# Performance work log

Hardware: AMD Instinct MI355X
Metric: run time of the kernel (lower is better)

## Reference

```python
import jax, jax.numpy as jnp
import numpy as np

IN_DIM, HID, OUT = 256, 10, 50
LEN_S = 4096
GAUSSIAN_DEGREE = 1


def _pdist2(a, b):
    # squared pairwise L2 distance, clamped at 0
    an = jnp.sum(a * a, axis=1)[:, None]
    bn = jnp.sum(b * b, axis=1)[None, :]
    d = an + bn - 2.0 * (a @ b.T)
    return jnp.maximum(d, 0.0)


def _mlp(x, W1, b1, W2, b2, W3, b3, W4, b4):
    h = jax.nn.softplus(x @ W1 + b1)
    h = jax.nn.softplus(h @ W2 + b2)
    h = jax.nn.softplus(h @ W3 + b3)
    return h @ W4 + b4


def setup_inputs() -> dict:
    key = jax.random.key(0)
    ks = jax.random.split(key, 12)
    inp = {
        "X": jax.random.normal(ks[0], (LEN_S, IN_DIM), jnp.float32),
        "Y": jax.random.normal(ks[1], (LEN_S, IN_DIM), jnp.float32),
        "W1": jax.random.normal(ks[2], (IN_DIM, HID), jnp.float32) / np.sqrt(IN_DIM),
        "b1": jnp.zeros((HID,), jnp.float32),
        "W2": jax.random.normal(ks[3], (HID, HID), jnp.float32) / np.sqrt(HID),
        "b2": jnp.zeros((HID,), jnp.float32),
        "W3": jax.random.normal(ks[4], (HID, HID), jnp.float32) / np.sqrt(HID),
        "b3": jnp.zeros((HID,), jnp.float32),
        "W4": jax.random.normal(ks[5], (HID, OUT), jnp.float32) / np.sqrt(HID),
        "b4": jnp.zeros((OUT,), jnp.float32),
        "epsilon_opt": jnp.array(np.log(5e-11), jnp.float32),
        "sigma_q_opt": jnp.array(np.sqrt(2 * 32 * 32), jnp.float32),
        "sigma_phi_opt": jnp.array(np.sqrt(0.005), jnp.float32),
    }
    return inp


def _deep_mmd(X, Y, W1, b1, W2, b2, W3, b3, W4, b4, epsilon_opt, sigma_q_opt, sigma_phi_opt):
    feats_org = jnp.concatenate([X, Y], axis=0)
    feats = _mlp(feats_org, W1, b1, W2, b2, W3, b3, W4, b4)
    epsilon = jax.nn.sigmoid(epsilon_opt)
    sigma_q = sigma_q_opt ** 2
    sigma_phi = sigma_phi_opt ** 2

    nx = ny = LEN_S
    x, y = feats[:nx], feats[nx:]
    xo, yo = feats_org[:nx], feats_org[nx:]

    def kernel(a, b, ao, bo):
        d = _pdist2(a, b)
        do = _pdist2(ao, bo)
        smooth = jnp.exp(-((d / sigma_phi) ** GAUSSIAN_DEGREE) - do / sigma_q)
        return (1.0 - epsilon) * smooth + epsilon * jnp.exp(-do / sigma_q)

    k_x = kernel(x, x, xo, xo)
    k_y = kernel(y, y, yo, yo)
    k_xy = kernel(x, y, xo, yo)

    # unbiased MMD estimate
    xx = (jnp.sum(k_x) - jnp.trace(k_x)) / (nx * (nx - 1))
    yy = (jnp.sum(k_y) - jnp.trace(k_y)) / (ny * (ny - 1))
    xy = (jnp.sum(k_xy) - jnp.trace(k_xy)) / (nx * (ny - 1))
    mmd2 = xx - 2.0 * xy + yy

    # variance estimate
    h = k_x + k_y - k_xy - k_xy.T
    hs = jnp.sum(h, axis=1)
    v1 = (4.0 / ny ** 3) * jnp.dot(hs, hs)
    v2 = (4.0 / nx ** 4) * jnp.sum(h) ** 2
    var = v1 - v2 + 1e-8
    return jnp.stack([mmd2, var])


def reference(X, Y, W1, b1, W2, b2, W3, b3, W4, b4, epsilon_opt, sigma_q_opt, sigma_phi_opt):
    return _deep_mmd(X, Y, W1, b1, W2, b2, W3, b3, W4, b4, epsilon_opt, sigma_q_opt, sigma_phi_opt)
```

## Files before the change

### kernel.cpp

```cpp
#include <hip/hip_runtime.h>
#include <math.h>


#define N_S 4096
#define LOG2E 1.4426950408889634

typedef _Float16 v8h __attribute__((ext_vector_type(8)));
typedef float v16f __attribute__((ext_vector_type(16)));

union U16 { uint4 u; v8h h; };

__device__ __forceinline__ void pack_hilo(const float* fv, uint4* hi, uint4* lo) {
    U16 H, L;
#pragma unroll
    for (int u = 0; u < 8; ++u) {
        _Float16 h = (_Float16)fv[u];
        H.h[u] = h;
        L.h[u] = (_Float16)(fv[u] - (float)h);
    }
    *hi = H.u; *lo = L.u;
}

__device__ __forceinline__ uint4 pack_hi(const float* fv) {
    U16 H;
#pragma unroll
    for (int u = 0; u < 8; ++u) H.h[u] = (_Float16)fv[u];
    return H.u;
}

__device__ __forceinline__ void gload16(const void* g, void* lds) {
    __builtin_amdgcn_global_load_lds(
        (const __attribute__((address_space(1))) unsigned int*)g,
        (__attribute__((address_space(3))) unsigned int*)lds, 16, 0, 0);
}

__global__ __launch_bounds__(256)
void mlp_kernel(const float* __restrict__ X, const float* __restrict__ Y,
                const float* __restrict__ W1, const float* __restrict__ b1,
                const float* __restrict__ W2, const float* __restrict__ b2,
                const float* __restrict__ W3, const float* __restrict__ b3,
                const float* __restrict__ W4, const float* __restrict__ b4,
                const float* __restrict__ sq,
                uint4* __restrict__ PKT, float* __restrict__ normF,
                float* __restrict__ wOrg,
                float* __restrict__ D8, double* __restrict__ S)
{
    __shared__ double sW1[8 * 330];
    __shared__ double sW2[100], sW3[100], sW4[500];
    __shared__ double sb1[10], sb2[10], sb3[10], sb4[50];
    int tid = threadIdx.x;
    int gt = blockIdx.x * 256 + tid;

    if (gt < 8192) D8[gt] = 0.0f;
    else if (gt < 8196) S[gt - 8192] = 0.0;

    {
        int kg = tid >> 5, kl = tid & 31;
#pragma unroll
        for (int j = 0; j < 10; ++j)
            sW1[kg * 330 + kl * 10 + j] = (double)W1[tid * 10 + j];
    }
    for (int i = tid; i < 100; i += 256) { sW2[i] = (double)W2[i]; sW3[i] = (double)W3[i]; }
    for (int i = tid; i < 500; i += 256) sW4[i] = (double)W4[i];
    if (tid < 10) { sb1[tid] = (double)b1[tid]; sb2[tid] = (double)b2[tid]; sb3[tid] = (double)b3[tid]; }
    if (tid < 50) sb4[tid] = (double)b4[tid];
    __syncthreads();

    int r = gt >> 3, g = gt & 7;
    const float* xr = (r < N_S) ? (X + (size_t)r * 256) : (Y + (size_t)(r - N_S) * 256);
    const float* xrg = xr + g * 32;
    const double* w1g = sW1 + g * 330;

    float xl[32];
    double z[10];
#pragma unroll
    for (int j = 0; j < 10; ++j) z[j] = 0.0;
    double nrm = 0.0;
    for (int k4 = 0; k4 < 32; k4 += 4) {
        float4 xv4 = *(const float4*)(xrg + k4);
        xl[k4] = xv4.x; xl[k4 + 1] = xv4.y; xl[k4 + 2] = xv4.z; xl[k4 + 3] = xv4.w;
        double xv[4] = {(double)xv4.x, (double)xv4.y, (double)xv4.z, (double)xv4.w};
#pragma unroll
        for (int u = 0; u < 4; ++u) {
            nrm += xv[u] * xv[u];
#pragma unroll
            for (int j = 0; j < 10; ++j) z[j] += xv[u] * w1g[(k4 + u) * 10 + j];
        }
    }
    {
#pragma unroll
        for (int u = 0; u < 4; ++u)
            PKT[(size_t)(g * 4 + u) * 8192 + r] = pack_hi(&xl[u * 8]);
    }

#pragma unroll
    for (int off = 1; off < 8; off <<= 1) {
        nrm += __shfl_xor(nrm, off);
#pragma unroll
        for (int j = 0; j < 10; ++j) z[j] += __shfl_xor(z[j], off);
    }
#pragma unroll
    for (int j = 0; j < 10; ++j) z[j] += sb1[j];
#pragma unroll
    for (int j = 0; j < 10; ++j) z[j] = fmax(z[j], 0.0) + log1p(exp(-fabs(z[j])));

    double z2[10];
#pragma unroll
    for (int j = 0; j < 10; ++j) z2[j] = sb2[j];
#pragma unroll
    for (int k = 0; k < 10; ++k)
#pragma unroll
        for (int j = 0; j < 10; ++j) z2[j] += z[k] * sW2[k * 10 + j];
#pragma unroll
    for (int j = 0; j < 10; ++j) z2[j] = fmax(z2[j], 0.0) + log1p(exp(-fabs(z2[j])));

    double z3[10];
#pragma unroll
    for (int j = 0; j < 10; ++j) z3[j] = sb3[j];
#pragma unroll
    for (int k = 0; k < 10; ++k)
#pragma unroll
        for (int j = 0; j < 10; ++j) z3[j] += z2[k] * sW3[k * 10 + j];
#pragma unroll
    for (int j = 0; j < 10; ++j) z3[j] = fmax(z3[j], 0.0) + log1p(exp(-fabs(z3[j])));

    double nf = 0.0;
    float ff[8];
#pragma unroll
    for (int u = 0; u < 8; ++u) ff[u] = 0.0f;
#pragma unroll
    for (int j = 0; j < 50; ++j) {
        double f = sb4[j];
#pragma unroll
        for (int k = 0; k < 10; ++k) f += z3[k] * sW4[k * 50 + j];
        nf += f * f;
        if ((j >> 3) == g) ff[j & 7] = (float)f;
    }
    {
        uint4 hi, lo;
        pack_hilo(ff, &hi, &lo);
        int colh = 32 + (g >> 2) * 8 + (g & 3);
        PKT[(size_t)colh * 8192 + r] = hi;
        PKT[(size_t)(colh + 4) * 8192 + r] = lo;
    }

    if (g == 0) {
        double sqv = (double)sq[0];
        double co = LOG2E / (sqv * sqv);
        wOrg[r] = (float)exp2(-nrm * co);
    }
    if (g == 1) normF[r] = (float)nf;
}

__device__ __forceinline__ v8h ldsm(const uint4* buf, int s, int g) {
    U16 t; t.u = buf[g * 128 + s];
    return t.h;
}

__global__ __launch_bounds__(512, 4)
void pair_kernel(const uint4* __restrict__ PKT, const float* __restrict__ normF,
                 const float* __restrict__ wOrg,
                 const float* __restrict__ ep, const float* __restrict__ sq,
                 const float* __restrict__ sph,
                 float* __restrict__ D8, double* __restrict__ S)
{
    __shared__ __align__(16) char smem[65536];

    int tid = threadIdx.x;
    int lane = tid & 63, w = tid >> 6;
    int wr2 = w >> 2, wc4 = w & 3;

    int orig = blockIdx.x;
    int L = (orig & 7) * 260 + (orig >> 3);
    int it = (int)((129.0 - sqrt(16641.0 - 8.0 * (double)L)) * 0.5);
    while (it * (129 - it) / 2 > L) --it;
    while ((it + 1) * (128 - it) / 2 <= L) ++it;
    int jt = it + (L - it * (129 - it) / 2);
    int i0 = it * 128, j0 = jt * 128;

    auto stage = [&](int t, int hb) {
        char* Ab = smem + hb * 32768;
        char* Bb = Ab + 16384;
        int soff = (t < 4) ? t * 8 : 32 + (t - 4) * 8;
#pragma unroll
        for (int i = 0; i < 2; ++i) {
            int u = i * 512 + tid;
            int row = u & 127, s8 = u >> 7;
            const uint4* ga = &PKT[(size_t)(soff + s8) * 8192 + i0 + row];
            const uint4* gb = &PKT[(size_t)(soff + s8) * 8192 + j0 + row];
            char* la = Ab + (i * 512 + (w << 6)) * 16;
            char* lb = Bb + (i * 512 + (w << 6)) * 16;
            gload16(ga, la);
            gload16(gb, lb);
        }
    };

    stage(0, 0);

    bool sameHalf = (jt < 32) || (it >= 32);
    bool isDiag = (it == jt);
    bool isTrace = (jt == it + 32);
    int region = (jt < 32) ? 0 : ((it >= 32) ? 1 : 2);
    float sgn = sameHalf ? 1.0f : -1.0f;

    int rs0 = wr2 * 64 + (lane & 31), rs1 = rs0 + 32;
    int cs = wc4 * 32 + (lane & 31);

    auto mfma_org = [&](int hb, v16f& a0, v16f& a1) {
        const uint4* Ab = (const uint4*)(smem + hb * 32768);
        const uint4* Bb = (const uint4*)(smem + hb * 32768 + 16384);
#pragma unroll
        for (int ks = 0; ks < 4; ++ks) {
            int gl = ks * 2 + (lane >> 5);
            v8h ah0 = ldsm(Ab, rs0, gl), ah1 = ldsm(Ab, rs1, gl);
            v8h bh = ldsm(Bb, cs, gl);
            a0 = __builtin_amdgcn_mfma_f32_32x32x16_f16(ah0, bh, a0, 0, 0, 0);
            a1 = __builtin_amdgcn_mfma_f32_32x32x16_f16(ah1, bh, a1, 0, 0, 0);
        }
    };
    auto mfma_feat = [&](int hb, v16f& a0, v16f& a1) {
        const uint4* Ab = (const uint4*)(smem + hb * 32768);
        const uint4* Bb = (const uint4*)(smem + hb * 32768 + 16384);
#pragma unroll
        for (int ks = 0; ks < 2; ++ks) {
            int gl = ks * 2 + (lane >> 5);
            v8h ah0 = ldsm(Ab, rs0, gl), ah1 = ldsm(Ab, rs1, gl);
            v8h al0 = ldsm(Ab, rs0, 4 + gl), al1 = ldsm(Ab, rs1, 4 + gl);
            v8h bh = ldsm(Bb, cs, gl), bl = ldsm(Bb, cs, 4 + gl);
            a0 = __builtin_amdgcn_mfma_f32_32x32x16_f16(al0, bh, a0, 0, 0, 0);
            a0 = __builtin_amdgcn_mfma_f32_32x32x16_f16(ah0, bl, a0, 0, 0, 0);
            a0 = __builtin_amdgcn_mfma_f32_32x32x16_f16(ah0, bh, a0, 0, 0, 0);
            a1 = __builtin_amdgcn_mfma_f32_32x32x16_f16(al1, bh, a1, 0, 0, 0);
            a1 = __builtin_amdgcn_mfma_f32_32x32x16_f16(ah1, bl, a1, 0, 0, 0);
            a1 = __builtin_amdgcn_mfma_f32_32x32x16_f16(ah1, bh, a1, 0, 0, 0);
        }
    };

    v16f accG0{}, accG1{}, accF0{}, accF1{};

#pragma unroll
    for (int t = 0; t < 6; ++t) {
        int hb = t & 1;
        asm volatile("s_waitcnt vmcnt(0)" ::: "memory");
        __builtin_amdgcn_sched_barrier(0);
        __builtin_amdgcn_s_barrier();
        __builtin_amdgcn_sched_barrier(0);
        if (t < 5) stage(t + 1, hb ^ 1);
        __builtin_amdgcn_s_setprio(1);
        if (t < 4) mfma_org(hb, accG0, accG1);
        else       mfma_feat(hb, accF0, accF1);
        __builtin_amdgcn_s_setprio(0);
    }
    __syncthreads();

    double epd = (double)ep[0];
    double eps = 1.0 / (1.0 + exp(-epd));
    double sqv = (double)sq[0], spv = (double)sph[0];
    float cf = (float)(LOG2E / (spv * spv));
    float twoco = (float)(2.0 * LOG2E / (sqv * sqv));
    float epsv = (float)eps, ome = (float)(1.0 - eps);

    float* E2 = (float*)smem;

    double bsum = 0.0, trsum = 0.0;
    float colacc = 0.0f;
    int cl = wc4 * 32 + (lane & 31);
    float wb = wOrg[j0 + cl];
    float nbF = normF[j0 + cl];

    auto evalacc = [&](const v16f& aG, const v16f& aF, int rbase) {
        float4 wa4[4], na4[4];
#pragma unroll
        for (int q = 0; q < 4; ++q) {
            int rb = i0 + rbase + 4 * (lane >> 5) + 8 * q;
            wa4[q] = *(const float4*)&wOrg[rb];
            na4[q] = *(const float4*)&normF[rb];
        }
#pragma unroll
        for (int reg = 0; reg < 16; ++reg) {
            int rl = rbase + 4 * (lane >> 5) + (reg & 3) + 8 * (reg >> 2);
            float wa = ((const float*)&wa4[reg >> 2])[reg & 3];
            float naA = ((const float*)&na4[reg >> 2])[reg & 3];
            float dfeat = fmaxf(naA + nbF - 2.0f * aF[reg], 0.0f);
            float e2v = exp2f(-dfeat * cf);
            float kv = wa * wb * exp2f(aG[reg] * twoco) * (ome * e2v + epsv);
            if (isDiag && rl == cl) kv = 0.0f;
            if (isTrace && cl == rl) trsum += (double)kv;
            bsum += (double)kv;
            colacc += kv;
            E2[rl * 128 + cl] = kv;
        }
    };
    evalacc(accG0, accF0, wr2 * 64);
    evalacc(accG1, accF1, wr2 * 64 + 32);
    __syncthreads();

    {
        int row = tid >> 2, q = tid & 3;
        int rot = ((q << 1) | (row & 1));
        float s = 0.0f;
#pragma unroll
        for (int c = 0; c < 8; ++c) {
            int cc = (c + rot) & 7;
            float4 v = *(const float4*)&E2[row * 128 + q * 32 + cc * 4];
            s += v.x + v.y + v.z + v.w;
        }
        s += __shfl_xor(s, 1);
        s += __shfl_xor(s, 2);
        if (q == 0) atomicAdd(&D8[i0 + row], sgn * s);
    }

    if (!isDiag) {
        atomicAdd(&D8[j0 + cl], sgn * colacc);
    }

#pragma unroll
    for (int off = 32; off > 0; off >>= 1) bsum += __shfl_down(bsum, off);
    if (isTrace) {
#pragma unroll
        for (int off = 32; off > 0; off >>= 1) trsum += __shfl_down(trsum, off);
    }
    __syncthreads();
    double* dred = (double*)smem;
    if (lane == 0) { dred[w] = bsum; dred[8 + w] = trsum; }
    __syncthreads();
    if (tid == 0) {
        double wgt = (sameHalf && !isDiag) ? 2.0 : 1.0;
        double t0 = 0.0, t1 = 0.0;
#pragma unroll
        for (int q = 0; q < 8; ++q) { t0 += dred[q]; t1 += dred[8 + q]; }
        atomicAdd(&S[region], wgt * t0);
        if (isTrace) atomicAdd(&S[3], t1);
    }
}

__global__ __launch_bounds__(256)
void final_kernel(const float* __restrict__ D8, const double* __restrict__ S,
                  float* __restrict__ out)
{
    __shared__ double buf[512];
    int tid = threadIdx.x;
    double sD = 0, sD2 = 0;
    for (int i = tid; i < 4096; i += 256) {
        double d = (double)D8[i] + (double)D8[i + 4096];
        sD += d; sD2 += d * d;
    }
    buf[tid] = sD; buf[256 + tid] = sD2;
    __syncthreads();
    for (int s = 128; s > 0; s >>= 1) {
        if (tid < s) { buf[tid] += buf[tid + s]; buf[256 + tid] += buf[256 + tid + s]; }
        __syncthreads();
    }
    if (tid == 0) {
        double n = (double)N_S, D = n * (n - 1.0);
        double xx = S[0] / D, yy = S[1] / D, xy = (S[2] - S[3]) / D;
        double mmd2 = xx - 2.0 * xy + yy;
        double sumd = buf[0], sumd2 = buf[256];
        double sumh = 2.0 * n + sumd;
        double sumhs2 = 4.0 * n + 4.0 * sumd + sumd2;
        double n3 = n * n * n, n4 = n3 * n;
        double var = 4.0 / n3 * sumhs2 - 4.0 / n4 * sumh * sumh + 1e-8;
        out[0] = (float)mmd2;
        out[1] = (float)var;
    }
}

extern "C" void kernel_launch(void* const* d_in, const int* in_sizes, int n_in,
                              void* d_out, int out_size, void* d_ws, size_t ws_size,
                              hipStream_t stream)
{
    const float* X   = (const float*)d_in[0];
    const float* Y   = (const float*)d_in[1];
    const float* W1  = (const float*)d_in[2];
    const float* b1  = (const float*)d_in[3];
    const float* W2  = (const float*)d_in[4];
    const float* b2  = (const float*)d_in[5];
    const float* W3  = (const float*)d_in[6];
    const float* b3  = (const float*)d_in[7];
    const float* W4  = (const float*)d_in[8];
    const float* b4  = (const float*)d_in[9];
    const float* ep  = (const float*)d_in[10];
    const float* sq  = (const float*)d_in[11];
    const float* sph = (const float*)d_in[12];
    float* out = (float*)d_out;

    char* ws = (char*)d_ws;
    uint4*  PKT   = (uint4*)ws;
    float*  wOrg  = (float*)(ws + 6291456);
    float*  normF = (float*)(ws + 6324224);
    float*  D8    = (float*)(ws + 6356992);
    double* S     = (double*)(ws + 6389760);

    mlp_kernel<<<256, 256, 0, stream>>>(X, Y, W1, b1, W2, b2, W3, b3, W4, b4,
                                        sq, PKT, normF, wOrg, D8, S);

    pair_kernel<<<2080, 512, 0, stream>>>(PKT, normF, wOrg, ep, sq, sph, D8, S);

    final_kernel<<<1, 256, 0, stream>>>(D8, S, out);
}
```

Before: 182.5 us.

## Use 4 waves per block with 64x64 warp tiles in pair kernel

Shrinks the pair kernel block from 8 waves to 4 and gives each wave a 64x64 sub-tile with four accumulators per product instead of 64x32 with two. Each wave reuses its A and B fragment loads across more MFMAs, so fewer LDS reads are needed per MFMA, and the staging loop and reductions are adjusted to match. In exchange each wave holds more accumulator registers and fewer waves are resident per block to hide latency, and the 64KB of shared memory per block still limits occupancy.

```diff
diff --git a/kernel.cpp b/kernel.cpp
--- a/kernel.cpp
+++ b/kernel.cpp
@@ -157,7 +157,7 @@
     return t.h;
 }
 
-__global__ __launch_bounds__(512, 4)
+__global__ __launch_bounds__(256, 2)
 void pair_kernel(const uint4* __restrict__ PKT, const float* __restrict__ normF,
                  const float* __restrict__ wOrg,
                  const float* __restrict__ ep, const float* __restrict__ sq,
@@ -168,7 +168,7 @@
 
     int tid = threadIdx.x;
     int lane = tid & 63, w = tid >> 6;
-    int wr2 = w >> 2, wc4 = w & 3;
+    int wr = w >> 1, wc = w & 1;
 
     int orig = blockIdx.x;
     int L = (orig & 7) * 260 + (orig >> 3);
@@ -183,13 +183,13 @@
         char* Bb = Ab + 16384;
         int soff = (t < 4) ? t * 8 : 32 + (t - 4) * 8;
 #pragma unroll
-        for (int i = 0; i < 2; ++i) {
-            int u = i * 512 + tid;
+        for (int i = 0; i < 4; ++i) {
+            int u = i * 256 + tid;
             int row = u & 127, s8 = u >> 7;
             const uint4* ga = &PKT[(size_t)(soff + s8) * 8192 + i0 + row];
             const uint4* gb = &PKT[(size_t)(soff + s8) * 8192 + j0 + row];
-            char* la = Ab + (i * 512 + (w << 6)) * 16;
-            char* lb = Bb + (i * 512 + (w << 6)) * 16;
+            char* la = Ab + (i * 256 + (w << 6)) * 16;
+            char* lb = Bb + (i * 256 + (w << 6)) * 16;
             gload16(ga, la);
             gload16(gb, lb);
         }
@@ -203,22 +203,24 @@
     int region = (jt < 32) ? 0 : ((it >= 32) ? 1 : 2);
     float sgn = sameHalf ? 1.0f : -1.0f;
 
-    int rs0 = wr2 * 64 + (lane & 31), rs1 = rs0 + 32;
-    int cs = wc4 * 32 + (lane & 31);
-
-    auto mfma_org = [&](int hb, v16f& a0, v16f& a1) {
+    int rs0 = wr * 64 + (lane & 31), rs1 = rs0 + 32;
+    int cs0 = wc * 64 + (lane & 31), cs1 = cs0 + 32;
+
+    auto mfma_org = [&](int hb, v16f& a00, v16f& a01, v16f& a10, v16f& a11) {
         const uint4* Ab = (const uint4*)(smem + hb * 32768);
         const uint4* Bb = (const uint4*)(smem + hb * 32768 + 16384);
 #pragma unroll
         for (int ks = 0; ks < 4; ++ks) {
             int gl = ks * 2 + (lane >> 5);
             v8h ah0 = ldsm(Ab, rs0, gl), ah1 = ldsm(Ab, rs1, gl);
-            v8h bh = ldsm(Bb, cs, gl);
-            a0 = __builtin_amdgcn_mfma_f32_32x32x16_f16(ah0, bh, a0, 0, 0, 0);
-            a1 = __builtin_amdgcn_mfma_f32_32x32x16_f16(ah1, bh, a1, 0, 0, 0);
+            v8h bh0 = ldsm(Bb, cs0, gl), bh1 = ldsm(Bb, cs1, gl);
+            a00 = __builtin_amdgcn_mfma_f32_32x32x16_f16(ah0, bh0, a00, 0, 0, 0);
+            a01 = __builtin_amdgcn_mfma_f32_32x32x16_f16(ah0, bh1, a01, 0, 0, 0);
+            a10 = __builtin_amdgcn_mfma_f32_32x32x16_f16(ah1, bh0, a10, 0, 0, 0);
+            a11 = __builtin_amdgcn_mfma_f32_32x32x16_f16(ah1, bh1, a11, 0, 0, 0);
         }
     };
-    auto mfma_feat = [&](int hb, v16f& a0, v16f& a1) {
+    auto mfma_feat = [&](int hb, v16f& a00, v16f& a01, v16f& a10, v16f& a11) {
         const uint4* Ab = (const uint4*)(smem + hb * 32768);
         const uint4* Bb = (const uint4*)(smem + hb * 32768 + 16384);
 #pragma unroll
@@ -226,17 +228,25 @@
             int gl = ks * 2 + (lane >> 5);
             v8h ah0 = ldsm(Ab, rs0, gl), ah1 = ldsm(Ab, rs1, gl);
             v8h al0 = ldsm(Ab, rs0, 4 + gl), al1 = ldsm(Ab, rs1, 4 + gl);
-            v8h bh = ldsm(Bb, cs, gl), bl = ldsm(Bb, cs, 4 + gl);
-            a0 = __builtin_amdgcn_mfma_f32_32x32x16_f16(al0, bh, a0, 0, 0, 0);
-            a0 = __builtin_amdgcn_mfma_f32_32x32x16_f16(ah0, bl, a0, 0, 0, 0);
-            a0 = __builtin_amdgcn_mfma_f32_32x32x16_f16(ah0, bh, a0, 0, 0, 0);
-            a1 = __builtin_amdgcn_mfma_f32_32x32x16_f16(al1, bh, a1, 0, 0, 0);
-            a1 = __builtin_amdgcn_mfma_f32_32x32x16_f16(ah1, bl, a1, 0, 0, 0);
-            a1 = __builtin_amdgcn_mfma_f32_32x32x16_f16(ah1, bh, a1, 0, 0, 0);
+            v8h bh0 = ldsm(Bb, cs0, gl), bh1 = ldsm(Bb, cs1, gl);
+            v8h bl0 = ldsm(Bb, cs0, 4 + gl), bl1 = ldsm(Bb, cs1, 4 + gl);
+            a00 = __builtin_amdgcn_mfma_f32_32x32x16_f16(al0, bh0, a00, 0, 0, 0);
+            a00 = __builtin_amdgcn_mfma_f32_32x32x16_f16(ah0, bl0, a00, 0, 0, 0);
+            a00 = __builtin_amdgcn_mfma_f32_32x32x16_f16(ah0, bh0, a00, 0, 0, 0);
+            a01 = __builtin_amdgcn_mfma_f32_32x32x16_f16(al0, bh1, a01, 0, 0, 0);
+            a01 = __builtin_amdgcn_mfma_f32_32x32x16_f16(ah0, bl1, a01, 0, 0, 0);
+            a01 = __builtin_amdgcn_mfma_f32_32x32x16_f16(ah0, bh1, a01, 0, 0, 0);
+            a10 = __builtin_amdgcn_mfma_f32_32x32x16_f16(al1, bh0, a10, 0, 0, 0);
+            a10 = __builtin_amdgcn_mfma_f32_32x32x16_f16(ah1, bl0, a10, 0, 0, 0);
+            a10 = __builtin_amdgcn_mfma_f32_32x32x16_f16(ah1, bh0, a10, 0, 0, 0);
+            a11 = __builtin_amdgcn_mfma_f32_32x32x16_f16(al1, bh1, a11, 0, 0, 0);
+            a11 = __builtin_amdgcn_mfma_f32_32x32x16_f16(ah1, bl1, a11, 0, 0, 0);
+            a11 = __builtin_amdgcn_mfma_f32_32x32x16_f16(ah1, bh1, a11, 0, 0, 0);
         }
     };
 
-    v16f accG0{}, accG1{}, accF0{}, accF1{};
+    v16f aG00{}, aG01{}, aG10{}, aG11{};
+    v16f aF00{}, aF01{}, aF10{}, aF11{};
 
 #pragma unroll
     for (int t = 0; t < 6; ++t) {
@@ -247,8 +257,8 @@
         __builtin_amdgcn_sched_barrier(0);
         if (t < 5) stage(t + 1, hb ^ 1);
         __builtin_amdgcn_s_setprio(1);
-        if (t < 4) mfma_org(hb, accG0, accG1);
-        else       mfma_feat(hb, accF0, accF1);
+        if (t < 4) mfma_org(hb, aG00, aG01, aG10, aG11);
+        else       mfma_feat(hb, aF00, aF01, aF10, aF11);
         __builtin_amdgcn_s_setprio(0);
     }
     __syncthreads();
@@ -263,12 +273,13 @@
     float* E2 = (float*)smem;
 
     double bsum = 0.0, trsum = 0.0;
-    float colacc = 0.0f;
-    int cl = wc4 * 32 + (lane & 31);
-    float wb = wOrg[j0 + cl];
-    float nbF = normF[j0 + cl];
-
-    auto evalacc = [&](const v16f& aG, const v16f& aF, int rbase) {
+    float colacc0 = 0.0f, colacc1 = 0.0f;
+    int cl0 = wc * 64 + (lane & 31), cl1 = cl0 + 32;
+    float wb0 = wOrg[j0 + cl0], nb0 = normF[j0 + cl0];
+    float wb1 = wOrg[j0 + cl1], nb1 = normF[j0 + cl1];
+
+    auto evalrow = [&](const v16f& g0, const v16f& f0,
+                       const v16f& g1, const v16f& f1, int rbase) {
         float4 wa4[4], na4[4];
 #pragma unroll
         for (int q = 0; q < 4; ++q) {
@@ -281,37 +292,48 @@
             int rl = rbase + 4 * (lane >> 5) + (reg & 3) + 8 * (reg >> 2);
             float wa = ((const float*)&wa4[reg >> 2])[reg & 3];
             float naA = ((const float*)&na4[reg >> 2])[reg & 3];
-            float dfeat = fmaxf(naA + nbF - 2.0f * aF[reg], 0.0f);
-            float e2v = exp2f(-dfeat * cf);
-            float kv = wa * wb * exp2f(aG[reg] * twoco) * (ome * e2v + epsv);
-            if (isDiag && rl == cl) kv = 0.0f;
-            if (isTrace && cl == rl) trsum += (double)kv;
-            bsum += (double)kv;
-            colacc += kv;
-            E2[rl * 128 + cl] = kv;
+            {
+                float dfeat = fmaxf(naA + nb0 - 2.0f * f0[reg], 0.0f);
+                float e2v = exp2f(-dfeat * cf);
+                float kv = wa * wb0 * exp2f(g0[reg] * twoco) * (ome * e2v + epsv);
+                if (isDiag && rl == cl0) kv = 0.0f;
+                if (isTrace && cl0 == rl) trsum += (double)kv;
+                bsum += (double)kv;
+                colacc0 += kv;
+                E2[rl * 128 + cl0] = kv;
+            }
+            {
+                float dfeat = fmaxf(naA + nb1 - 2.0f * f1[reg], 0.0f);
+                float e2v = exp2f(-dfeat * cf);
+                float kv = wa * wb1 * exp2f(g1[reg] * twoco) * (ome * e2v + epsv);
+                if (isDiag && rl == cl1) kv = 0.0f;
+                if (isTrace && cl1 == rl) trsum += (double)kv;
+                bsum += (double)kv;
+                colacc1 += kv;
+                E2[rl * 128 + cl1] = kv;
+            }
         }
     };
-    evalacc(accG0, accF0, wr2 * 64);
-    evalacc(accG1, accF1, wr2 * 64 + 32);
+    evalrow(aG00, aF00, aG01, aF01, wr * 64);
+    evalrow(aG10, aF10, aG11, aF11, wr * 64 + 32);
     __syncthreads();
 
     {
-        int row = tid >> 2, q = tid & 3;
-        int rot = ((q << 1) | (row & 1));
+        int row = tid >> 1, half = tid & 1;
         float s = 0.0f;
 #pragma unroll
-        for (int c = 0; c < 8; ++c) {
-            int cc = (c + rot) & 7;
-            float4 v = *(const float4*)&E2[row * 128 + q * 32 + cc * 4];
+        for (int c = 0; c < 16; ++c) {
+            int cc = (c + row) & 15;
+            float4 v = *(const float4*)&E2[row * 128 + half * 64 + cc * 4];
             s += v.x + v.y + v.z + v.w;
         }
         s += __shfl_xor(s, 1);
-        s += __shfl_xor(s, 2);
-        if (q == 0) atomicAdd(&D8[i0 + row], sgn * s);
+        if (half == 0) atomicAdd(&D8[i0 + row], sgn * s);
     }
 
     if (!isDiag) {
-        atomicAdd(&D8[j0 + cl], sgn * colacc);
+        atomicAdd(&D8[j0 + cl0], sgn * colacc0);
+        atomicAdd(&D8[j0 + cl1], sgn * colacc1);
     }
 
 #pragma unroll
@@ -322,15 +344,12 @@
     }
     __syncthreads();
     double* dred = (double*)smem;
-    if (lane == 0) { dred[w] = bsum; dred[8 + w] = trsum; }
+    if (lane == 0) { dred[w] = bsum; dred[4 + w] = trsum; }
     __syncthreads();
     if (tid == 0) {
         double wgt = (sameHalf && !isDiag) ? 2.0 : 1.0;
-        double t0 = 0.0, t1 = 0.0;
-#pragma unroll
-        for (int q = 0; q < 8; ++q) { t0 += dred[q]; t1 += dred[8 + q]; }
-        atomicAdd(&S[region], wgt * t0);
-        if (isTrace) atomicAdd(&S[3], t1);
+        atomicAdd(&S[region], wgt * (dred[0] + dred[1] + dred[2] + dred[3]));
+        if (isTrace) atomicAdd(&S[3], dred[4] + dred[5] + dred[6] + dred[7]);
     }
 }
 
@@ -394,7 +413,7 @@
     mlp_kernel<<<256, 256, 0, stream>>>(X, Y, W1, b1, W2, b2, W3, b3, W4, b4,
                                         sq, PKT, normF, wOrg, D8, S);
 
-    pair_kernel<<<2080, 512, 0, stream>>>(PKT, normF, wOrg, ep, sq, sph, D8, S);
+    pair_kernel<<<2080, 256, 0, stream>>>(PKT, normF, wOrg, ep, sq, sph, D8, S);
 
     final_kernel<<<1, 256, 0, stream>>>(D8, S, out);
 }
```

New measurement: 174.8 us. 4.2% less time.

## Split MLP rows across 16 threads and distribute hidden-layer neurons per lane

Applied to the files above, without the earlier changes.

The MLP kernel now assigns 16 threads per input row instead of 8, halving the per-thread slice of the first-layer dot product and doubling the grid. The small hidden layers are no longer computed redundantly by every thread. Each lane now computes one neuron and broadcasts it through wavefront shuffles, and the output layer's 50 features are split across 8 lanes with a shuffle reduction for the feature norm. This targets the serial fp64 work and latency in the MLP prologue, at the cost of more shuffles and idle lanes (g>=10).

```diff
diff --git a/kernel.cpp b/kernel.cpp
--- a/kernel.cpp
+++ b/kernel.cpp
@@ -45,7 +45,7 @@
                 float* __restrict__ wOrg,
                 float* __restrict__ D8, double* __restrict__ S)
 {
-    __shared__ double sW1[8 * 330];
+    __shared__ double sW1[16 * 161];
     __shared__ double sW2[100], sW3[100], sW4[500];
     __shared__ double sb1[10], sb2[10], sb3[10], sb4[50];
     int tid = threadIdx.x;
@@ -55,10 +55,10 @@
     else if (gt < 8196) S[gt - 8192] = 0.0;
 
     {
-        int kg = tid >> 5, kl = tid & 31;
+        int kg = tid >> 4, kl = tid & 15;
 #pragma unroll
         for (int j = 0; j < 10; ++j)
-            sW1[kg * 330 + kl * 10 + j] = (double)W1[tid * 10 + j];
+            sW1[kg * 161 + kl * 10 + j] = (double)W1[tid * 10 + j];
     }
     for (int i = tid; i < 100; i += 256) { sW2[i] = (double)W2[i]; sW3[i] = (double)W3[i]; }
     for (int i = tid; i < 500; i += 256) sW4[i] = (double)W4[i];
@@ -66,17 +66,19 @@
     if (tid < 50) sb4[tid] = (double)b4[tid];
     __syncthreads();
 
-    int r = gt >> 3, g = gt & 7;
+    int r = gt >> 4, g = gt & 15;
+    int lane = tid & 63;
+    int base16 = lane & 48;
     const float* xr = (r < N_S) ? (X + (size_t)r * 256) : (Y + (size_t)(r - N_S) * 256);
-    const float* xrg = xr + g * 32;
-    const double* w1g = sW1 + g * 330;
-
-    float xl[32];
+    const float* xrg = xr + g * 16;
+    const double* w1g = sW1 + g * 161;
+
+    float xl[16];
     double z[10];
 #pragma unroll
     for (int j = 0; j < 10; ++j) z[j] = 0.0;
     double nrm = 0.0;
-    for (int k4 = 0; k4 < 32; k4 += 4) {
+    for (int k4 = 0; k4 < 16; k4 += 4) {
         float4 xv4 = *(const float4*)(xrg + k4);
         xl[k4] = xv4.x; xl[k4 + 1] = xv4.y; xl[k4 + 2] = xv4.z; xl[k4 + 3] = xv4.w;
         double xv[4] = {(double)xv4.x, (double)xv4.y, (double)xv4.z, (double)xv4.w};
@@ -89,54 +91,67 @@
     }
     {
 #pragma unroll
-        for (int u = 0; u < 4; ++u)
-            PKT[(size_t)(g * 4 + u) * 8192 + r] = pack_hi(&xl[u * 8]);
-    }
-
-#pragma unroll
-    for (int off = 1; off < 8; off <<= 1) {
+        for (int u = 0; u < 2; ++u)
+            PKT[(size_t)(g * 2 + u) * 8192 + r] = pack_hi(&xl[u * 8]);
+    }
+
+#pragma unroll
+    for (int off = 1; off < 16; off <<= 1) {
         nrm += __shfl_xor(nrm, off);
 #pragma unroll
         for (int j = 0; j < 10; ++j) z[j] += __shfl_xor(z[j], off);
     }
-#pragma unroll
-    for (int j = 0; j < 10; ++j) z[j] += sb1[j];
-#pragma unroll
-    for (int j = 0; j < 10; ++j) z[j] = fmax(z[j], 0.0) + log1p(exp(-fabs(z[j])));
-
-    double z2[10];
-#pragma unroll
-    for (int j = 0; j < 10; ++j) z2[j] = sb2[j];
-#pragma unroll
-    for (int k = 0; k < 10; ++k)
-#pragma unroll
-        for (int j = 0; j < 10; ++j) z2[j] += z[k] * sW2[k * 10 + j];
-#pragma unroll
-    for (int j = 0; j < 10; ++j) z2[j] = fmax(z2[j], 0.0) + log1p(exp(-fabs(z2[j])));
-
-    double z3[10];
-#pragma unroll
-    for (int j = 0; j < 10; ++j) z3[j] = sb3[j];
-#pragma unroll
-    for (int k = 0; k < 10; ++k)
-#pragma unroll
-        for (int j = 0; j < 10; ++j) z3[j] += z2[k] * sW3[k * 10 + j];
-#pragma unroll
-    for (int j = 0; j < 10; ++j) z3[j] = fmax(z3[j], 0.0) + log1p(exp(-fabs(z3[j])));
+
+    double sp = 0.0;
+    if (g < 10) {
+        double s = z[g] + sb1[g];
+        sp = fmax(s, 0.0) + log1p(exp(-fabs(s)));
+    }
+    double h1[10];
+#pragma unroll
+    for (int j = 0; j < 10; ++j) h1[j] = __shfl(sp, base16 | j);
+
+    if (g < 10) {
+        double s = sb2[g];
+#pragma unroll
+        for (int k = 0; k < 10; ++k) s += h1[k] * sW2[k * 10 + g];
+        sp = fmax(s, 0.0) + log1p(exp(-fabs(s)));
+    }
+    double h2[10];
+#pragma unroll
+    for (int j = 0; j < 10; ++j) h2[j] = __shfl(sp, base16 | j);
+
+    if (g < 10) {
+        double s = sb3[g];
+#pragma unroll
+        for (int k = 0; k < 10; ++k) s += h2[k] * sW3[k * 10 + g];
+        sp = fmax(s, 0.0) + log1p(exp(-fabs(s)));
+    }
+    double h3[10];
+#pragma unroll
+    for (int j = 0; j < 10; ++j) h3[j] = __shfl(sp, base16 | j);
 
     double nf = 0.0;
     float ff[8];
 #pragma unroll
     for (int u = 0; u < 8; ++u) ff[u] = 0.0f;
-#pragma unroll
-    for (int j = 0; j < 50; ++j) {
-        double f = sb4[j];
-#pragma unroll
-        for (int k = 0; k < 10; ++k) f += z3[k] * sW4[k * 50 + j];
-        nf += f * f;
-        if ((j >> 3) == g) ff[j & 7] = (float)f;
-    }
-    {
+    if (g < 8) {
+#pragma unroll
+        for (int u = 0; u < 8; ++u) {
+            int j = 8 * g + u;
+            if (j < 50) {
+                double f = sb4[j];
+#pragma unroll
+                for (int k = 0; k < 10; ++k) f += h3[k] * sW4[k * 50 + j];
+                nf += f * f;
+                ff[u] = (float)f;
+            }
+        }
+    }
+#pragma unroll
+    for (int off = 1; off < 16; off <<= 1) nf += __shfl_xor(nf, off);
+
+    if (g < 8) {
         uint4 hi, lo;
         pack_hilo(ff, &hi, &lo);
         int colh = 32 + (g >> 2) * 8 + (g & 3);
@@ -391,7 +406,7 @@
     float*  D8    = (float*)(ws + 6356992);
     double* S     = (double*)(ws + 6389760);
 
-    mlp_kernel<<<256, 256, 0, stream>>>(X, Y, W1, b1, W2, b2, W3, b3, W4, b4,
+    mlp_kernel<<<512, 256, 0, stream>>>(X, Y, W1, b1, W2, b2, W3, b3, W4, b4,
                                         sq, PKT, normF, wOrg, D8, S);
 
     pair_kernel<<<2080, 512, 0, stream>>>(PKT, normF, wOrg, ep, sq, sph, D8, S);
```

Result: faster. 165.6 us (-9.2%).
